# Performance work log

Hardware: AMD Instinct MI355X
Metric: run time of the kernel (lower is better)

The kernel has to match this reference:

```python
import jax, jax.numpy as jnp
import numpy as np

# Instant-NGP / tcnn hash grid encoding constants (from init_kwargs)
L = 16           # n_levels
F = 2            # n_features_per_level
T = 2 ** 15      # hashmap size per level
DIM = 3
BASE = 16.0      # base_resolution
FINEST = 512.0   # finest_resolution
RANGE = 1.0
B = (FINEST / BASE) ** (1.0 / (L - 1))  # per_level_scale
N_POINTS = 500000
# tcnn spatial hash primes (first dim uses 1)
PRIMES = jnp.array([1, 2654435761, 805459861], dtype=jnp.uint32)


def setup_inputs() -> dict:
    key = jax.random.key(0)
    k1, k2 = jax.random.split(key)
    x = jax.random.uniform(k1, (N_POINTS, DIM), dtype=jnp.float32)  # points in [0,1)
    table = jax.random.normal(k2, (L, T, F), dtype=jnp.float32) * 1e-4  # tcnn-style tiny init
    return {"x": x, "table": table}


def reference(x, table):
    # wrapper: map from [-range, range] to [0, 1]
    xn = (x + RANGE) / (2.0 * RANGE)                       # [N, 3]
    n = xn.shape[0]
    # per-level grid scale (tcnn: scale = base * b^l - 1)
    scales = BASE * (B ** jnp.arange(L, dtype=jnp.float32)) - 1.0  # [L]
    pos = xn[:, None, :] * scales[None, :, None] + 0.5     # [N, L, 3]
    pos_floor = jnp.floor(pos)
    frac = pos - pos_floor                                  # [N, L, 3]
    grid = pos_floor.astype(jnp.uint32)                    # [N, L, 3]
    # 8 cube corners as binary offsets
    corners = jnp.array([[(c >> d) & 1 for d in range(DIM)] for c in range(2 ** DIM)],
                        dtype=jnp.uint32)                   # [8, 3]
    coords = grid[:, :, None, :] + corners[None, None, :, :]  # [N, L, 8, 3] uint32
    h = coords * PRIMES                                     # uint32 wraps (modular mult)
    idx = (h[..., 0] ^ h[..., 1] ^ h[..., 2]) & jnp.uint32(T - 1)  # [N, L, 8]
    # gather per-level features: [N, L, 8, F]
    feats = table[jnp.arange(L)[None, :, None], idx]
    # trilinear interpolation weights
    cf = corners.astype(jnp.float32)                        # [8, 3]
    w = jnp.prod(jnp.where(cf[None, None, :, :] == 1.0,
                           frac[:, :, None, :],
                           1.0 - frac[:, :, None, :]), axis=-1)  # [N, L, 8]
    out = jnp.einsum('nlc,nlcf->nlf', w, feats)             # [N, L, F]
    return out.reshape(n, L * F)
```

## Files before the change

kernel.cpp:

```cpp
#include <hip/hip_runtime.h>
#include <hip/hip_fp16.h>
#include <stdint.h>


constexpr int      kL  = 16;
constexpr int      kT  = 32768;
constexpr uint32_t kM  = kT - 1;
constexpr uint32_t kP1 = 2654435761u;
constexpr uint32_t kP2 = 805459861u;
constexpr int      kNC = 16;
constexpr int      kBT = 1024;

typedef float f32x2 __attribute__((ext_vector_type(2)));
typedef __attribute__((address_space(3))) uint32_t u32_lds;

__device__ __constant__ float c_scales[kL] = {
    15.0f,
    19.158736798317972f,
    24.398416831491190f,
    31.0f,
    39.317473596635944f,
    49.796833662982380f,
    63.0f,
    79.634947193271890f,
    100.59366732596477f,
    127.0f,
    160.26989438654378f,
    202.18733465192953f,
    255.0f,
    321.53978877308750f,
    405.37466930385903f,
    511.0f
};

__device__ __forceinline__ void load3(float (&v)[3], const float* __restrict__ x, int n) {
    v[0] = x[n * 3 + 0];
    v[1] = x[n * 3 + 1];
    v[2] = x[n * 3 + 2];
}

__device__ __forceinline__ void hash_addr(
    uint32_t lbase, float s, const float (&xv)[3],
    float (&fr)[3], uint32_t (&adr)[8])
{
    float p0 = fmaf((xv[0] + 1.0f) * 0.5f, s, 0.5f);
    float p1 = fmaf((xv[1] + 1.0f) * 0.5f, s, 0.5f);
    float p2 = fmaf((xv[2] + 1.0f) * 0.5f, s, 0.5f);

    float fl0 = floorf(p0), fl1 = floorf(p1), fl2 = floorf(p2);
    fr[0] = p0 - fl0;  fr[1] = p1 - fl1;  fr[2] = p2 - fl2;

    uint32_t g0 = (uint32_t)(int)fl0;
    uint32_t g1 = (uint32_t)(int)fl1;
    uint32_t g2 = (uint32_t)(int)fl2;

    uint32_t g0p = g0 + 1u;
    uint32_t hy0 = g1 * kP1;  uint32_t hy1 = hy0 + kP1;
    uint32_t hz0 = g2 * kP2;  uint32_t hz1 = hz0 + kP2;

    uint32_t hyz0 = hy0 ^ hz0;
    uint32_t hyz1 = hy1 ^ hz0;
    uint32_t hyz2 = hy0 ^ hz1;
    uint32_t hyz3 = hy1 ^ hz1;

    adr[0] = lbase + (((g0  ^ hyz0) & kM) << 2);
    adr[1] = lbase + (((g0p ^ hyz0) & kM) << 2);
    adr[2] = lbase + (((g0  ^ hyz1) & kM) << 2);
    adr[3] = lbase + (((g0p ^ hyz1) & kM) << 2);
    adr[4] = lbase + (((g0  ^ hyz2) & kM) << 2);
    adr[5] = lbase + (((g0p ^ hyz2) & kM) << 2);
    adr[6] = lbase + (((g0  ^ hyz3) & kM) << 2);
    adr[7] = lbase + (((g0p ^ hyz3) & kM) << 2);
}

__device__ __forceinline__ void issue_asm8(const uint32_t (&adr)[8], uint32_t (&e)[8]) {
    asm volatile(
        "ds_read_b32 %0, %8\n\t"
        "ds_read_b32 %1, %9\n\t"
        "ds_read_b32 %2, %10\n\t"
        "ds_read_b32 %3, %11\n\t"
        "ds_read_b32 %4, %12\n\t"
        "ds_read_b32 %5, %13\n\t"
        "ds_read_b32 %6, %14\n\t"
        "ds_read_b32 %7, %15"
        : "=&v"(e[0]), "=&v"(e[1]), "=&v"(e[2]), "=&v"(e[3]),
          "=&v"(e[4]), "=&v"(e[5]), "=&v"(e[6]), "=&v"(e[7])
        : "v"(adr[0]), "v"(adr[1]), "v"(adr[2]), "v"(adr[3]),
          "v"(adr[4]), "v"(adr[5]), "v"(adr[6]), "v"(adr[7]));
}

__device__ __forceinline__ void weights8(const float (&fr)[3], float (&wf)[8]) {
    float wx0 = 1.0f - fr[0];
    float wy0 = 1.0f - fr[1];
    float wz0 = 1.0f - fr[2];
    float wyz0 = wy0   * wz0;
    float wyz1 = fr[1] * wz0;
    float wyz2 = wy0   * fr[2];
    float wyz3 = fr[1] * fr[2];
    wf[0] = wx0   * wyz0;  wf[1] = fr[0] * wyz0;
    wf[2] = wx0   * wyz1;  wf[3] = fr[0] * wyz1;
    wf[4] = wx0   * wyz2;  wf[5] = fr[0] * wyz2;
    wf[6] = wx0   * wyz3;  wf[7] = fr[0] * wyz3;
}

__device__ __forceinline__ f32x2 consume8(const uint32_t (&e)[8], const float (&wf)[8]) {
    __half2 acc = __float2half2_rn(0.0f);
#pragma unroll
    for (int cc = 0; cc < 8; ++cc) {
        __half2 h = *reinterpret_cast<const __half2*>(&e[cc]);
        acc = __hfma2(__float2half2_rn(wf[cc]), h, acc);
    }
    f32x2 r;
    r.x = __low2float(acc);
    r.y = __high2float(acc);
    return r;
}

__global__ __launch_bounds__(kBT, 4) void hashgrid_fwd(
    const float*  __restrict__ x,
    const float2* __restrict__ table,
    f32x2*        __restrict__ out,
    int n_points, int chunk_sz)
{
    __shared__ uint32_t ltab[kT];

    int bid = blockIdx.x;
    int l   = bid >> 4;
    int c   = bid & 15;

    const float4* tsrc4 = reinterpret_cast<const float4*>(table + (size_t)l * kT);
    for (int e = threadIdx.x; e < kT / 2; e += kBT) {
        float4 q = tsrc4[e];
        uint2 pp;
        pp.x = ((uint32_t)__half_as_ushort(__float2half_rn(q.y)) << 16)
             |  (uint32_t)__half_as_ushort(__float2half_rn(q.x));
        pp.y = ((uint32_t)__half_as_ushort(__float2half_rn(q.w)) << 16)
             |  (uint32_t)__half_as_ushort(__float2half_rn(q.z));
        *reinterpret_cast<uint2*>(&ltab[e * 2]) = pp;
    }
    __syncthreads();

    uint32_t lbase = (uint32_t)(uintptr_t)(u32_lds*)ltab;

    float s    = c_scales[l];
    int   tid  = (int)threadIdx.x;
    int   base = c * chunk_sz;
    int   lim  = min(base + chunk_sz, n_points);

    int unguarded = (chunk_sz / kBT) & ~1;

    int n = base + tid;
    float xc0[3], xc1[3];
    load3(xc0, x, n);
    load3(xc1, x, n + kBT);

    for (int it = 0; it < unguarded; it += 2) {
        float    fr0[3], fr1[3];
        uint32_t a0[8], a1[8];
        uint32_t e0[8], e1[8];

        hash_addr(lbase, s, xc0, fr0, a0);
        hash_addr(lbase, s, xc1, fr1, a1);
        issue_asm8(a0, e0);
        issue_asm8(a1, e1);
        __builtin_amdgcn_sched_barrier(0);

        float wf0[8], wf1[8];
        weights8(fr0, wf0);
        weights8(fr1, wf1);
        bool last = (it + 2 >= unguarded);
        int  np0  = last ? n : n + 2 * kBT;
        int  np1  = last ? n : n + 3 * kBT;
        load3(xc0, x, np0);
        load3(xc1, x, np1);

        asm volatile("s_waitcnt lgkmcnt(0)" ::: "memory");
        __builtin_amdgcn_sched_barrier(0);
        f32x2 r0 = consume8(e0, wf0);
        out[(size_t)n * kL + l] = r0;
        f32x2 r1 = consume8(e1, wf1);
        out[(size_t)(n + kBT) * kL + l] = r1;

        n += 2 * kBT;
    }

    for (int nG = base + tid + unguarded * kBT; nG < lim; nG += kBT) {
        float xv[3];
        load3(xv, x, nG);
        float frv[3]; uint32_t av[8], ev[8];
        hash_addr(lbase, s, xv, frv, av);
        issue_asm8(av, ev);
        float wfv[8];
        weights8(frv, wfv);
        asm volatile("s_waitcnt lgkmcnt(0)" ::: "memory");
        __builtin_amdgcn_sched_barrier(0);
        f32x2 r = consume8(ev, wfv);
        out[(size_t)nG * kL + l] = r;
    }
}

extern "C" void kernel_launch(void* const* d_in, const int* in_sizes, int n_in,
                              void* d_out, int out_size, void* d_ws, size_t ws_size,
                              hipStream_t stream) {
    const float*  x     = (const float*)d_in[0];
    const float2* table = (const float2*)d_in[1];
    f32x2*        out   = (f32x2*)d_out;

    int n_points = in_sizes[0] / 3;
    int chunk_sz = (n_points + kNC - 1) / kNC;
    int blocks   = kL * kNC;

    hashgrid_fwd<<<blocks, kBT, 0, stream>>>(x, table, out, n_points, chunk_sz);
}
```

Before: 50.14 us.

## Software-pipeline LDS hash gathers across iterations with partial lgkmcnt waits

Restructures the per-thread loop into a rolling software pipeline. Each step issues the 8 LDS reads for the next point before consuming the previous point's reads, and waits with lgkmcnt(8) instead of draining all outstanding LDS operations, so LDS latency overlaps with interpolation math. It also folds the coordinate normalisation into a single fma (x*A+C) and clamps prefetch indices so the tail is handled by a guarded final stage instead of a separate scalar loop. The risk is higher register pressure from keeping two in-flight gather sets, plus subtle correctness in the lgkmcnt counting, because the global x loads also use the lgkm counter on some paths.

```diff
diff --git a/kernel.cpp b/kernel.cpp
--- a/kernel.cpp
+++ b/kernel.cpp
@@ -33,19 +33,21 @@
     511.0f
 };
 
-__device__ __forceinline__ void load3(float (&v)[3], const float* __restrict__ x, int n) {
-    v[0] = x[n * 3 + 0];
-    v[1] = x[n * 3 + 1];
-    v[2] = x[n * 3 + 2];
+__device__ __forceinline__ void load3c(float (&v)[3], const float* __restrict__ x,
+                                       int n, int nmax) {
+    int m = min(n, nmax);
+    v[0] = x[m * 3 + 0];
+    v[1] = x[m * 3 + 1];
+    v[2] = x[m * 3 + 2];
 }
 
 __device__ __forceinline__ void hash_addr(
-    uint32_t lbase, float s, const float (&xv)[3],
+    uint32_t lbase, float A, float C, const float (&xv)[3],
     float (&fr)[3], uint32_t (&adr)[8])
 {
-    float p0 = fmaf((xv[0] + 1.0f) * 0.5f, s, 0.5f);
-    float p1 = fmaf((xv[1] + 1.0f) * 0.5f, s, 0.5f);
-    float p2 = fmaf((xv[2] + 1.0f) * 0.5f, s, 0.5f);
+    float p0 = fmaf(xv[0], A, C);
+    float p1 = fmaf(xv[1], A, C);
+    float p2 = fmaf(xv[2], A, C);
 
     float fl0 = floorf(p0), fl1 = floorf(p1), fl2 = floorf(p2);
     fr[0] = p0 - fl0;  fr[1] = p1 - fl1;  fr[2] = p2 - fl2;
@@ -116,6 +118,42 @@
     return r;
 }
 
+template<bool GUARD>
+__device__ __forceinline__ void pipe_body(
+    uint32_t lbase, float A, float C,
+    const float* __restrict__ x, f32x2* __restrict__ out,
+    int n, int l, int lim, int nmax,
+    float (&frCur)[3], uint32_t (&eCur)[8],
+    const float (&xIss)[3], float (&frNew)[3], uint32_t (&eNew)[8],
+    float (&xPref)[3])
+{
+    uint32_t adr[8];
+    hash_addr(lbase, A, C, xIss, frNew, adr);
+    issue_asm8(adr, eNew);
+    __builtin_amdgcn_sched_barrier(0);
+
+    float wf[8];
+    weights8(frCur, wf);
+    load3c(xPref, x, n + 2 * kBT, nmax);
+
+    asm volatile("s_waitcnt lgkmcnt(8)" ::: "memory");
+    __builtin_amdgcn_sched_barrier(0);
+    f32x2 r = consume8(eCur, wf);
+    if (!GUARD || n < lim) out[(size_t)n * kL + l] = r;
+}
+
+__device__ __forceinline__ void epilogue(
+    const float (&fr)[3], const uint32_t (&e)[8],
+    f32x2* __restrict__ out, int n, int l, int lim)
+{
+    float wf[8];
+    weights8(fr, wf);
+    asm volatile("s_waitcnt lgkmcnt(0)" ::: "memory");
+    __builtin_amdgcn_sched_barrier(0);
+    f32x2 r = consume8(e, wf);
+    if (n < lim) out[(size_t)n * kL + l] = r;
+}
+
 __global__ __launch_bounds__(kBT, 4) void hashgrid_fwd(
     const float*  __restrict__ x,
     const float2* __restrict__ table,
@@ -142,60 +180,45 @@
 
     uint32_t lbase = (uint32_t)(uintptr_t)(u32_lds*)ltab;
 
-    float s    = c_scales[l];
-    int   tid  = (int)threadIdx.x;
-    int   base = c * chunk_sz;
-    int   lim  = min(base + chunk_sz, n_points);
-
-    int unguarded = (chunk_sz / kBT) & ~1;
+    float s = c_scales[l];
+    float A = s * 0.5f;
+    float C = fmaf(s, 0.5f, 0.5f);
+
+    int tid  = (int)threadIdx.x;
+    int base = c * chunk_sz;
+    int lim  = min(base + chunk_sz, n_points);
+    int nmax = n_points - 1;
+
+    int span  = lim - base;
+    int rows  = (span + kBT - 1) / kBT;
+    int main2 = (rows - 1) & ~1;
+
+    float    xA[3], xB[3], frA[3], frB[3];
+    uint32_t eA[8], eB[8];
 
     int n = base + tid;
-    float xc0[3], xc1[3];
-    load3(xc0, x, n);
-    load3(xc1, x, n + kBT);
-
-    for (int it = 0; it < unguarded; it += 2) {
-        float    fr0[3], fr1[3];
-        uint32_t a0[8], a1[8];
-        uint32_t e0[8], e1[8];
-
-        hash_addr(lbase, s, xc0, fr0, a0);
-        hash_addr(lbase, s, xc1, fr1, a1);
-        issue_asm8(a0, e0);
-        issue_asm8(a1, e1);
-        __builtin_amdgcn_sched_barrier(0);
-
-        float wf0[8], wf1[8];
-        weights8(fr0, wf0);
-        weights8(fr1, wf1);
-        bool last = (it + 2 >= unguarded);
-        int  np0  = last ? n : n + 2 * kBT;
-        int  np1  = last ? n : n + 3 * kBT;
-        load3(xc0, x, np0);
-        load3(xc1, x, np1);
-
-        asm volatile("s_waitcnt lgkmcnt(0)" ::: "memory");
-        __builtin_amdgcn_sched_barrier(0);
-        f32x2 r0 = consume8(e0, wf0);
-        out[(size_t)n * kL + l] = r0;
-        f32x2 r1 = consume8(e1, wf1);
-        out[(size_t)(n + kBT) * kL + l] = r1;
-
+    load3c(xA, x, n,       nmax);
+    load3c(xB, x, n + kBT, nmax);
+    {
+        uint32_t adr[8];
+        hash_addr(lbase, A, C, xA, frA, adr);
+        issue_asm8(adr, eA);
+    }
+
+    for (int r = 0; r < main2; r += 2) {
+        pipe_body<false>(lbase, A, C, x, out, n,       l, lim, nmax,
+                         frA, eA, xB, frB, eB, xA);
+        pipe_body<false>(lbase, A, C, x, out, n + kBT, l, lim, nmax,
+                         frB, eB, xA, frA, eA, xB);
         n += 2 * kBT;
     }
 
-    for (int nG = base + tid + unguarded * kBT; nG < lim; nG += kBT) {
-        float xv[3];
-        load3(xv, x, nG);
-        float frv[3]; uint32_t av[8], ev[8];
-        hash_addr(lbase, s, xv, frv, av);
-        issue_asm8(av, ev);
-        float wfv[8];
-        weights8(frv, wfv);
-        asm volatile("s_waitcnt lgkmcnt(0)" ::: "memory");
-        __builtin_amdgcn_sched_barrier(0);
-        f32x2 r = consume8(ev, wfv);
-        out[(size_t)nG * kL + l] = r;
+    if (main2 != rows - 1) {
+        pipe_body<true>(lbase, A, C, x, out, n, l, lim, nmax,
+                        frA, eA, xB, frB, eB, xA);
+        epilogue(frB, eB, out, n + kBT, l, lim);
+    } else {
+        epilogue(frA, eA, out, n, l, lim);
     }
 }
 
```

Result: no change. 50.73 us (+1.2%).
